# Kernel tuning notes

Hardware: AMD Instinct MI355X
Metric: run time of the kernel (lower is better)

The kernel has to match this reference:

```python
import jax, jax.numpy as jnp
import numpy as np

N = 50000      # num nodes
E = 800000     # num edges
IN = 512       # in_feats (= num_hidden)
H = 8          # num_heads
D = 64         # out_feats per head (H*D = 512)
NEG_SLOPE = 0.2


def setup_inputs() -> dict:
    key = jax.random.key(0)
    ks = jax.random.split(key, 7)
    feat = jax.random.normal(ks[0], (N, IN), jnp.float32)
    src = jax.random.randint(ks[1], (E,), 0, N)
    dst = jax.random.randint(ks[2], (E,), 0, N)
    W_fc = jax.random.normal(ks[3], (IN, H * D), jnp.float32) * (1.0 / np.sqrt(IN))
    W_res = jax.random.normal(ks[4], (IN, H * D), jnp.float32) * (1.0 / np.sqrt(IN))
    attn_l = jax.random.normal(ks[5], (1, H, D), jnp.float32) * 0.1
    attn_r = jax.random.normal(ks[6], (1, H, D), jnp.float32) * 0.1
    return {"feat": feat, "src": src, "dst": dst, "W_fc": W_fc,
            "W_res": W_res, "attn_l": attn_l, "attn_r": attn_r}


def reference(feat, src, dst, W_fc, W_res, attn_l, attn_r):
    # fc: [N, IN] @ [IN, H*D] -> [N, H, D]
    ft = (feat @ W_fc).reshape(N, H, D)
    # attention logits per node: el = sum(ft * attn_l, -1), er likewise -> [N, H]
    el = jnp.sum(ft * attn_l, axis=-1)
    er = jnp.sum(ft * attn_r, axis=-1)
    # u_add_v on edges, then LeakyReLU -> [E, H]
    e = jax.nn.leaky_relu(el[src] + er[dst], negative_slope=NEG_SLOPE)
    # edge_softmax: normalize over incoming edges of each dst node
    m = jax.ops.segment_max(e, dst, num_segments=N)            # [N, H]
    m = jnp.where(jnp.isfinite(m), m, jnp.zeros_like(m))       # guard zero-in-degree
    ex = jnp.exp(e - m[dst])                                   # [E, H]
    s = jax.ops.segment_sum(ex, dst, num_segments=N)           # [N, H]
    a = ex / jnp.maximum(s[dst], 1e-9)                         # [E, H]
    # u_mul_e + sum aggregation: gather src features, weight, scatter-add to dst
    msg = ft[src] * a[:, :, None]                              # [E, H, D]
    rst = jax.ops.segment_sum(msg, dst, num_segments=N)        # [N, H, D]
    # residual: res_fc Linear since in_dst_feats != out_feats
    rst = rst + (feat @ W_res).reshape(N, H, D)
    return rst
```

## Files before the change

### kernel.cpp

```cpp
#include <hip/hip_runtime.h>
#include <hip/hip_bf16.h>

#define NN 50000
#define EE 800000
#define INF 512
#define HH 8
#define DD 64
#define HD 512
#define NTOT 1024

typedef unsigned short u16;
typedef u16 u16x8 __attribute__((ext_vector_type(8)));
typedef __bf16 bf16x8 __attribute__((ext_vector_type(8)));
typedef float f32x4 __attribute__((ext_vector_type(4)));

__device__ __forceinline__ float bf2f(u16 u) {
    return __uint_as_float(((unsigned)u) << 16);
}
__device__ __forceinline__ u16 f2bf(float f) {
    __hip_bfloat16 h = __float2bfloat16(f);
    return *reinterpret_cast<u16*>(&h);
}

__global__ __launch_bounds__(256) void sniff5_kernel(const u16* __restrict__ p0,
                                                     const u16* __restrict__ p1,
                                                     const u16* __restrict__ p2,
                                                     const u16* __restrict__ p3,
                                                     const u16* __restrict__ p4,
                                                     int* __restrict__ flags) {
    const u16* ps[5] = {p0, p1, p2, p3, p4};
    const u16* p = ps[blockIdx.x];
    __shared__ int bad;
    if (threadIdx.x == 0) bad = 0;
    __syncthreads();
    float v = fabsf(bf2f(p[2 * threadIdx.x]));
    if (!(v < 1e4f)) atomicAdd(&bad, 1);
    __syncthreads();
    if (threadIdx.x == 0) flags[blockIdx.x] = (bad >= 8) ? 1 : 0;
}

__global__ __launch_bounds__(256) void transpose_kernel(const void* __restrict__ in,
                                                        u16* __restrict__ out,
                                                        const int* __restrict__ flag) {
    __shared__ u16 tile[64][65];
    const int isf32 = *flag;
    int tr = (blockIdx.x & 7) * 64;
    int tc = (blockIdx.x >> 3) * 64;
    for (int idx = threadIdx.x; idx < 64 * 64; idx += 256) {
        int r = idx >> 6, c = idx & 63;
        int g = (tr + r) * 512 + tc + c;
        tile[r][c] = isf32 ? f2bf(((const float*)in)[g]) : ((const u16*)in)[g];
    }
    __syncthreads();
    for (int idx = threadIdx.x; idx < 64 * 64; idx += 256) {
        int r = idx >> 6, c = idx & 63;
        out[(tc + r) * 512 + tr + c] = tile[c][r];
    }
}

__global__ void zero_deg_kernel(int* __restrict__ deg) {
    int t = blockIdx.x * 256 + threadIdx.x;
    if (t < NN) deg[t] = 0;
}

__global__ void count_kernel(const int* __restrict__ dst, int* __restrict__ deg) {
    int e = blockIdx.x * 256 + threadIdx.x;
    if (e < EE) atomicAdd(&deg[dst[e]], 1);
}

#define SCAN_CH 49
__global__ __launch_bounds__(1024) void scan_kernel(const int* __restrict__ deg,
                                                    int* __restrict__ rowptr,
                                                    int* __restrict__ cursor) {
    __shared__ int sums[1024];
    int t = threadIdx.x;
    int base = t * SCAN_CH;
    int s = 0;
    for (int k = 0; k < SCAN_CH; ++k) {
        int i = base + k;
        if (i < NN) s += deg[i];
    }
    sums[t] = s;
    __syncthreads();
    for (int off = 1; off < 1024; off <<= 1) {
        int v = (t >= off) ? sums[t - off] : 0;
        __syncthreads();
        sums[t] += v;
        __syncthreads();
    }
    int run = (t == 0) ? 0 : sums[t - 1];
    for (int k = 0; k < SCAN_CH; ++k) {
        int i = base + k;
        if (i < NN) {
            rowptr[i] = run;
            cursor[i] = run;
            run += deg[i];
        }
    }
    if (t == 0) rowptr[NN] = EE;
}

__global__ void scatter_kernel(const int* __restrict__ src, const int* __restrict__ dst,
                               int* __restrict__ cursor, int* __restrict__ csr_src) {
    int e = blockIdx.x * 256 + threadIdx.x;
    if (e < EE) {
        int p = atomicAdd(&cursor[dst[e]], 1);
        csr_src[p] = src[e];
    }
}

#define TM 128
#define TN 128
#define BK 32
#define LDK 40

__global__ __launch_bounds__(256) void gemm_kernel(const void* __restrict__ A,
                                                   const u16* __restrict__ Wt,
                                                   u16* __restrict__ ft,
                                                   float* __restrict__ outf,
                                                   const int* __restrict__ flag) {
    __shared__ u16 As[TM * LDK];
    __shared__ u16 Bs[TN * LDK];
    const int isf32 = *flag;
    const int m0 = blockIdx.x * TM;
    const int n0 = blockIdx.y * TN;
    const int tid = threadIdx.x;
    const int lane = tid & 63;
    const int wave = tid >> 6;
    const int wr = (wave >> 1) * 64;
    const int wc = (wave & 1) * 64;
    const int lrow = lane & 15;
    const int quad = lane >> 4;

    f32x4 acc[4][4] = {};

    for (int k0 = 0; k0 < INF; k0 += BK) {
        __syncthreads();
#pragma unroll
        for (int it = 0; it < 2; ++it) {
            int chunk = tid + it * 256;
            int r = chunk >> 2;
            int c = (chunk & 3) * 8;
            int gr = m0 + r;
            u16x8 av = {0, 0, 0, 0, 0, 0, 0, 0};
            if (gr < NN) {
                if (isf32) {
                    const f32x4* ap = (const f32x4*)((const float*)A + gr * INF + k0 + c);
                    f32x4 f0 = ap[0], f1 = ap[1];
#pragma unroll
                    for (int j = 0; j < 4; ++j) { av[j] = f2bf(f0[j]); av[4 + j] = f2bf(f1[j]); }
                } else {
                    av = *(const u16x8*)((const u16*)A + gr * INF + k0 + c);
                }
            }
            *(u16x8*)(As + r * LDK + c) = av;
            *(u16x8*)(Bs + r * LDK + c) = *(const u16x8*)(Wt + (n0 + r) * INF + k0 + c);
        }
        __syncthreads();

        bf16x8 af[4], bfr[4];
#pragma unroll
        for (int mi = 0; mi < 4; ++mi)
            af[mi] = *(const bf16x8*)(As + (wr + mi * 16 + lrow) * LDK + quad * 8);
#pragma unroll
        for (int ni = 0; ni < 4; ++ni)
            bfr[ni] = *(const bf16x8*)(Bs + (wc + ni * 16 + lrow) * LDK + quad * 8);
#pragma unroll
        for (int mi = 0; mi < 4; ++mi)
#pragma unroll
            for (int ni = 0; ni < 4; ++ni)
                acc[mi][ni] = __builtin_amdgcn_mfma_f32_16x16x32_bf16(af[mi], bfr[ni],
                                                                      acc[mi][ni], 0, 0, 0);
    }

#pragma unroll
    for (int mi = 0; mi < 4; ++mi) {
        int rb = m0 + wr + mi * 16 + quad * 4;
#pragma unroll
        for (int ni = 0; ni < 4; ++ni) {
            int col = n0 + wc + ni * 16 + lrow;
#pragma unroll
            for (int r = 0; r < 4; ++r) {
                int row = rb + r;
                if (row < NN) {
                    float v = acc[mi][ni][r];
                    if (col < HD) ft[row * HD + col] = f2bf(v);
                    else outf[row * HD + (col - HD)] = v;
                }
            }
        }
    }
}

__global__ __launch_bounds__(256) void attn_dot_kernel(const u16* __restrict__ ft,
                                                       const void* __restrict__ al,
                                                       const void* __restrict__ ar,
                                                       float* __restrict__ el,
                                                       float* __restrict__ er,
                                                       const int* __restrict__ flags) {
    int node = blockIdx.x * 4 + (threadIdx.x >> 6);
    int lane = threadIdx.x & 63;
    if (node >= NN) return;
    const int alf32 = flags[3];
    const int arf32 = flags[4];
    const u16* f = ft + node * HD;
#pragma unroll
    for (int h = 0; h < HH; ++h) {
        int i = h * 64 + lane;
        float wl = alf32 ? ((const float*)al)[i] : bf2f(((const u16*)al)[i]);
        float wr_ = arf32 ? ((const float*)ar)[i] : bf2f(((const u16*)ar)[i]);
        float x = bf2f(f[i]);
        float vl = x * wl;
        float vr = x * wr_;
#pragma unroll
        for (int off = 32; off > 0; off >>= 1) {
            vl += __shfl_down(vl, off);
            vr += __shfl_down(vr, off);
        }
        if (lane == 0) {
            el[node * HH + h] = vl;
            er[node * HH + h] = vr;
        }
    }
}

__global__ __launch_bounds__(256) void aggregate_kernel(const int* __restrict__ rowptr,
                                                        const int* __restrict__ csr_src,
                                                        const u16* __restrict__ ft,
                                                        const float* __restrict__ el,
                                                        const float* __restrict__ er,
                                                        float* __restrict__ outf) {
    int node = blockIdx.x * 4 + (threadIdx.x >> 6);
    if (node >= NN) return;
    int lane = threadIdx.x & 63;
    int head = lane >> 3;
    int beg = rowptr[node], end = rowptr[node + 1];
    float erd = er[node * HH + head];

    float m = -INFINITY;
    for (int i = beg; i < end; ++i) {
        int s = csr_src[i];
        float v = el[s * HH + head] + erd;
        v = v > 0.0f ? v : 0.2f * v;
        m = fmaxf(m, v);
    }

    float acc[8] = {};
    float sden = 0.0f;
    for (int i = beg; i < end; ++i) {
        int s = csr_src[i];
        float v = el[s * HH + head] + erd;
        v = v > 0.0f ? v : 0.2f * v;
        float ex = __expf(v - m);
        sden += ex;
        u16x8 f = *(const u16x8*)(ft + s * HD + lane * 8);
#pragma unroll
        for (int j = 0; j < 8; ++j) acc[j] += bf2f(f[j]) * ex;
    }

    float inv = 1.0f / fmaxf(sden, 1e-9f);
    float* op = outf + node * HD + lane * 8;
    f32x4 r0 = *(const f32x4*)op;
    f32x4 r1 = *(const f32x4*)(op + 4);
    f32x4 o0, o1;
#pragma unroll
    for (int j = 0; j < 4; ++j) {
        o0[j] = acc[j] * inv + r0[j];
        o1[j] = acc[4 + j] * inv + r1[j];
    }
    *(f32x4*)op = o0;
    *(f32x4*)(op + 4) = o1;
}

extern "C" void kernel_launch(void* const* d_in, const int* in_sizes, int n_in,
                              void* d_out, int out_size, void* d_ws, size_t ws_size,
                              hipStream_t stream) {
    const void* feat   = d_in[0];
    const int*  src    = (const int*)d_in[1];
    const int*  dst    = (const int*)d_in[2];
    const void* W_fc   = d_in[3];
    const void* W_res  = d_in[4];
    const void* attn_l = d_in[5];
    const void* attn_r = d_in[6];
    float* outf = (float*)d_out;

    char* ws = (char*)d_ws;
    int*   flags   = (int*)(ws);
    u16*   Wt      = (u16*)(ws + 256);
    u16*   ft      = (u16*)(ws + 1048832);
    float* el      = (float*)(ws + 52248832);
    float* er      = (float*)(ws + 53848832);
    int*   deg     = (int*)(ws + 55448832);
    int*   rowptr  = (int*)(ws + 55648832);
    int*   cursor  = (int*)(ws + 55848896);
    int*   csr_src = (int*)(ws + 56048896);

    sniff5_kernel<<<5, 256, 0, stream>>>((const u16*)feat, (const u16*)W_fc,
                                         (const u16*)W_res, (const u16*)attn_l,
                                         (const u16*)attn_r, flags);
    transpose_kernel<<<64, 256, 0, stream>>>(W_fc, Wt, flags + 1);
    transpose_kernel<<<64, 256, 0, stream>>>(W_res, Wt + 512 * 512, flags + 2);

    zero_deg_kernel<<<(NN + 255) / 256, 256, 0, stream>>>(deg);
    count_kernel<<<(EE + 255) / 256, 256, 0, stream>>>(dst, deg);
    scan_kernel<<<1, 1024, 0, stream>>>(deg, rowptr, cursor);
    scatter_kernel<<<(EE + 255) / 256, 256, 0, stream>>>(src, dst, cursor, csr_src);

    dim3 gg((NN + TM - 1) / TM, NTOT / TN);
    gemm_kernel<<<gg, 256, 0, stream>>>(feat, Wt, ft, outf, flags + 0);

    attn_dot_kernel<<<(NN + 3) / 4, 256, 0, stream>>>(ft, attn_l, attn_r, el, er, flags);
    aggregate_kernel<<<(NN + 3) / 4, 256, 0, stream>>>(rowptr, csr_src, ft, el, er, outf);
}
```

Measured before the change: 769.1 us.

## Use online softmax in aggregation, vectorize attention dot, remap GEMM blocks

The aggregation kernel's two passes over incoming edges (max, then exp-weighted sum) become one pass using an online-softmax rescale, with a one-step software prefetch of the next source's el and feature row. The attention-dot kernel now loads 8 contiguous elements per lane and reduces with xor-shuffles within groups of 8 lanes, instead of looping over heads with full-wave reductions. The GEMM grid is flattened so the 8 column tiles of one row block run next to each other, improving L2 reuse of the A rows. Online softmax adds extra exp calls and a multiply on each accumulator per edge in exchange for reading each edge's data only once.

```diff
diff --git a/kernel.cpp b/kernel.cpp
--- a/kernel.cpp
+++ b/kernel.cpp
@@ -122,8 +122,9 @@
     __shared__ u16 As[TM * LDK];
     __shared__ u16 Bs[TN * LDK];
     const int isf32 = *flag;
-    const int m0 = blockIdx.x * TM;
-    const int n0 = blockIdx.y * TN;
+    const int bid = blockIdx.x;
+    const int m0 = (bid >> 3) * TM;
+    const int n0 = (bid & 7) * TN;
     const int tid = threadIdx.x;
     const int lane = tid & 63;
     const int wave = tid >> 6;
@@ -199,28 +200,48 @@
                                                        float* __restrict__ er,
                                                        const int* __restrict__ flags) {
     int node = blockIdx.x * 4 + (threadIdx.x >> 6);
+    if (node >= NN) return;
     int lane = threadIdx.x & 63;
-    if (node >= NN) return;
-    const int alf32 = flags[3];
-    const int arf32 = flags[4];
-    const u16* f = ft + node * HD;
-#pragma unroll
-    for (int h = 0; h < HH; ++h) {
-        int i = h * 64 + lane;
-        float wl = alf32 ? ((const float*)al)[i] : bf2f(((const u16*)al)[i]);
-        float wr_ = arf32 ? ((const float*)ar)[i] : bf2f(((const u16*)ar)[i]);
-        float x = bf2f(f[i]);
-        float vl = x * wl;
-        float vr = x * wr_;
-#pragma unroll
-        for (int off = 32; off > 0; off >>= 1) {
-            vl += __shfl_down(vl, off);
-            vr += __shfl_down(vr, off);
-        }
-        if (lane == 0) {
-            el[node * HH + h] = vl;
-            er[node * HH + h] = vr;
-        }
+    int off = lane * 8;
+
+    float wl[8], wr_[8];
+    if (flags[3]) {
+        f32x4 a0 = *(const f32x4*)((const float*)al + off);
+        f32x4 a1 = *(const f32x4*)((const float*)al + off + 4);
+#pragma unroll
+        for (int j = 0; j < 4; ++j) { wl[j] = a0[j]; wl[4 + j] = a1[j]; }
+    } else {
+        u16x8 a = *(const u16x8*)((const u16*)al + off);
+#pragma unroll
+        for (int j = 0; j < 8; ++j) wl[j] = bf2f(a[j]);
+    }
+    if (flags[4]) {
+        f32x4 a0 = *(const f32x4*)((const float*)ar + off);
+        f32x4 a1 = *(const f32x4*)((const float*)ar + off + 4);
+#pragma unroll
+        for (int j = 0; j < 4; ++j) { wr_[j] = a0[j]; wr_[4 + j] = a1[j]; }
+    } else {
+        u16x8 a = *(const u16x8*)((const u16*)ar + off);
+#pragma unroll
+        for (int j = 0; j < 8; ++j) wr_[j] = bf2f(a[j]);
+    }
+
+    u16x8 f = *(const u16x8*)(ft + node * HD + off);
+    float vl = 0.0f, vr = 0.0f;
+#pragma unroll
+    for (int j = 0; j < 8; ++j) {
+        float x = bf2f(f[j]);
+        vl += x * wl[j];
+        vr += x * wr_[j];
+    }
+#pragma unroll
+    for (int msk = 1; msk < 8; msk <<= 1) {
+        vl += __shfl_xor(vl, msk);
+        vr += __shfl_xor(vr, msk);
+    }
+    if ((lane & 7) == 0) {
+        el[node * HH + (lane >> 3)] = vl;
+        er[node * HH + (lane >> 3)] = vr;
     }
 }
 
@@ -238,24 +259,33 @@
     float erd = er[node * HH + head];
 
     float m = -INFINITY;
+    float sden = 0.0f;
+    float acc[8] = {};
+
+    float el_n = 0.0f;
+    u16x8 f_n = {};
+    if (beg < end) {
+        int s0 = csr_src[beg];
+        el_n = el[s0 * HH + head];
+        f_n = *(const u16x8*)(ft + s0 * HD + lane * 8);
+    }
     for (int i = beg; i < end; ++i) {
-        int s = csr_src[i];
-        float v = el[s * HH + head] + erd;
+        float elv = el_n;
+        u16x8 f = f_n;
+        if (i + 1 < end) {
+            int s2 = csr_src[i + 1];
+            el_n = el[s2 * HH + head];
+            f_n = *(const u16x8*)(ft + s2 * HD + lane * 8);
+        }
+        float v = elv + erd;
         v = v > 0.0f ? v : 0.2f * v;
-        m = fmaxf(m, v);
-    }
-
-    float acc[8] = {};
-    float sden = 0.0f;
-    for (int i = beg; i < end; ++i) {
-        int s = csr_src[i];
-        float v = el[s * HH + head] + erd;
-        v = v > 0.0f ? v : 0.2f * v;
-        float ex = __expf(v - m);
-        sden += ex;
-        u16x8 f = *(const u16x8*)(ft + s * HD + lane * 8);
-#pragma unroll
-        for (int j = 0; j < 8; ++j) acc[j] += bf2f(f[j]) * ex;
+        float nm = fmaxf(m, v);
+        float scale = __expf(m - nm);
+        float ex = __expf(v - nm);
+        m = nm;
+        sden = sden * scale + ex;
+#pragma unroll
+        for (int j = 0; j < 8; ++j) acc[j] = acc[j] * scale + bf2f(f[j]) * ex;
     }
 
     float inv = 1.0f / fmaxf(sden, 1e-9f);
@@ -306,8 +336,8 @@
     scan_kernel<<<1, 1024, 0, stream>>>(deg, rowptr, cursor);
     scatter_kernel<<<(EE + 255) / 256, 256, 0, stream>>>(src, dst, cursor, csr_src);
 
-    dim3 gg((NN + TM - 1) / TM, NTOT / TN);
-    gemm_kernel<<<gg, 256, 0, stream>>>(feat, Wt, ft, outf, flags + 0);
+    int nmblk = (NN + TM - 1) / TM;
+    gemm_kernel<<<nmblk * 8, 256, 0, stream>>>(feat, Wt, ft, outf, flags + 0);
 
     attn_dot_kernel<<<(NN + 3) / 4, 256, 0, stream>>>(ft, attn_l, attn_r, el, er, flags);
     aggregate_kernel<<<(NN + 3) / 4, 256, 0, stream>>>(rowptr, csr_src, ft, el, er, outf);
```

After: 722.5 us. 6.1% less time.
